# Performance work log

Hardware: AMD Instinct MI355X
Metric: run time of the kernel (lower is better)

## Reference

```python
import jax, jax.numpy as jnp
import numpy as np

M_SIGMA = 1.0 * 0.997 / 3.0  # args.m * 0.997 / 3


def setup_inputs() -> dict:
    key = jax.random.key(0)
    k1, k2 = jax.random.split(key)
    B, D = 64, 512        # batch (sketches+shapes), embedding dim
    P = 256               # points per cloud
    embeddings = jax.random.normal(k1, (B, D), dtype=jnp.float32)
    xyz = jax.random.normal(k2, (B, P, 3), dtype=jnp.float32)
    return {"embeddings": embeddings, "xyz": xyz}


def _chamfer_all_pairs(shapes):
    # shapes: [M, P, 3]. Returns cd[i, j] = chamfer(shapes[i], shapes[j]),
    # chamfer = mean_p min_q ||x_p - y_q||^2 + mean_q min_p ||x_p - y_q||^2
    sq = jnp.sum(shapes * shapes, axis=-1)                  # [M, P]
    inner = jnp.einsum('ipd,jqd->ijpq', shapes, shapes)     # [M, M, P, P]
    d2 = sq[:, None, :, None] + sq[None, :, None, :] - 2.0 * inner
    cd = jnp.min(d2, axis=3).mean(axis=2) + jnp.min(d2, axis=2).mean(axis=2)
    return cd  # [M, M]


def reference(embeddings, xyz):
    # L2-normalize embeddings along feature dim
    emb = embeddings / jnp.linalg.norm(embeddings, axis=1, keepdims=True)
    B = emb.shape[0]
    mb = B // 2
    shapes = xyz[mb:]                                       # [mb, P, 3]
    sketch_feat, shape_feat = emb[:mb], emb[mb:]            # [mb, D] each
    inner_dot = sketch_feat @ shape_feat.T                  # [mb, mb]
    cd = _chamfer_all_pairs(shapes)                         # [mb, mb]
    real_dist = (cd ** 2) / (2.0 * M_SIGMA ** 2)
    p = jax.nn.softmax(-real_dist, axis=1)
    p_hat = jax.nn.softmax(inner_dot, axis=1)               # use_softmax=True
    reg = jnp.mean(jnp.abs(p_hat - p))                      # use_KL=False
    return reg
```

## Files before the change

### kernel.cpp

```cpp
#include <hip/hip_runtime.h>
#include <math.h>


typedef float f32x2 __attribute__((ext_vector_type(2)));

__device__ __forceinline__ float waveReduceSum64(float v) {
    #pragma unroll
    for (int m = 32; m > 0; m >>= 1) v += __shfl_xor(v, m, 64);
    return v;
}

__global__ __launch_bounds__(256) void pairs_kernel(const float* __restrict__ emb,
                                                    const float* __restrict__ xyz,
                                                    float* __restrict__ cdHalf,
                                                    float* __restrict__ dots) {
    const int t = threadIdx.x;
    const int b = blockIdx.x;

    __shared__ float S[512];

    if (b < 248) {
        const int w    = t >> 6;
        const int lane = t & 63;
        const int pairIdx = __builtin_amdgcn_readfirstlane((b << 2) | w);
        const int pb  = pairIdx >> 1;
        const int dir = pairIdx & 1;
        int ii = 0, rem = pb;
        while (rem >= (31 - ii)) { rem -= (31 - ii); ++ii; }
        const int jj = ii + 1 + rem;
        const int outer = dir ? jj : ii;
        const int inner = dir ? ii : jj;

        const float* Po = xyz + (32 + outer) * 768;
        const float* Qf = xyz + (32 + inner) * 768;

        float px[4], py[4], pz[4], pp[4];
        #pragma unroll
        for (int k = 0; k < 4; ++k) {
            const float* P = Po + 3 * (lane + 64 * k);
            px[k] = P[0]; py[k] = P[1]; pz[k] = P[2];
            pp[k] = px[k] * px[k] + py[k] * py[k] + pz[k] * pz[k];
        }
        const f32x2 X01 = {-2.f * px[0], -2.f * px[1]}, X23 = {-2.f * px[2], -2.f * px[3]};
        const f32x2 Y01 = {-2.f * py[0], -2.f * py[1]}, Y23 = {-2.f * py[2], -2.f * py[3]};
        const f32x2 Z01 = {-2.f * pz[0], -2.f * pz[1]}, Z23 = {-2.f * pz[2], -2.f * pz[3]};

        f32x2 m01 = {3.4e38f, 3.4e38f}, m23 = {3.4e38f, 3.4e38f};

        #pragma unroll 8
        for (int s = 0; s < 256; ++s) {
            const float qx = Qf[3 * s];
            const float qy = Qf[3 * s + 1];
            const float qz = Qf[3 * s + 2];
            const float qw = qx * qx + qy * qy + qz * qz;
            const f32x2 QX = {qx, qx}, QY = {qy, qy}, QZ = {qz, qz}, QW = {qw, qw};
            f32x2 e01 = Z01 * QZ + QW;
            e01 = Y01 * QY + e01;
            e01 = X01 * QX + e01;
            f32x2 e23 = Z23 * QZ + QW;
            e23 = Y23 * QY + e23;
            e23 = X23 * QX + e23;
            m01.x = fminf(m01.x, e01.x); m01.y = fminf(m01.y, e01.y);
            m23.x = fminf(m23.x, e23.x); m23.y = fminf(m23.y, e23.y);
        }

        float ssum = (m01.x + pp[0]) + (m01.y + pp[1]) +
                     (m23.x + pp[2]) + (m23.y + pp[3]);
        ssum = waveReduceSum64(ssum);
        if (lane == 0) cdHalf[pairIdx] = ssum * (1.0f / 256.0f);
    } else {
        const int i = b - 248;
        float* rowi = S;
        const float* Ei = emb + i * 512;
        rowi[t]       = Ei[t];
        rowi[t + 256] = Ei[t + 256];
        __syncthreads();

        const int w    = t >> 6;
        const int lane = t & 63;

        float ni = 0.0f;
        #pragma unroll
        for (int m = 0; m < 8; ++m) { float a = rowi[lane + 64 * m]; ni += a * a; }
        ni = waveReduceSum64(ni);

        for (int j = w; j < 32; j += 4) {
            const float* Ej = emb + (32 + j) * 512;
            float dot = 0.0f, nj = 0.0f;
            #pragma unroll
            for (int m = 0; m < 8; ++m) {
                float a  = rowi[lane + 64 * m];
                float bv = Ej[lane + 64 * m];
                dot += a * bv;
                nj  += bv * bv;
            }
            dot = waveReduceSum64(dot);
            nj  = waveReduceSum64(nj);
            if (lane == 0) dots[i * 32 + j] = dot * rsqrtf(ni * nj);
        }
    }
}

__global__ __launch_bounds__(1024) void finish_kernel(const float* __restrict__ cdHalf,
                                                      const float* __restrict__ dots,
                                                      float* __restrict__ out) {
    const int t = threadIdx.x;
    const int i = t >> 5;
    const int j = t & 31;
    const float inv_denom = 1.0f / (2.0f * (0.997f / 3.0f) * (0.997f / 3.0f));

    float c;
    if (i == j) {
        c = 0.0f;
    } else {
        const int a  = min(i, j), bb = max(i, j);
        const int pb = a * 31 - (a * (a - 1)) / 2 + (bb - a - 1);
        c = cdHalf[2 * pb] + cdHalf[2 * pb + 1];
    }
    float s = -(c * c) * inv_denom;
    float h = dots[t];

    float m1 = s;
    #pragma unroll
    for (int k = 16; k > 0; k >>= 1) m1 = fmaxf(m1, __shfl_xor(m1, k, 32));
    float e1 = expf(s - m1);
    float sum1 = e1;
    #pragma unroll
    for (int k = 16; k > 0; k >>= 1) sum1 += __shfl_xor(sum1, k, 32);
    float p = e1 / sum1;

    float m2 = h;
    #pragma unroll
    for (int k = 16; k > 0; k >>= 1) m2 = fmaxf(m2, __shfl_xor(m2, k, 32));
    float e2 = expf(h - m2);
    float sum2 = e2;
    #pragma unroll
    for (int k = 16; k > 0; k >>= 1) sum2 += __shfl_xor(sum2, k, 32);
    float ph = e2 / sum2;

    float a = fabsf(ph - p);
    a = waveReduceSum64(a);

    __shared__ float red[16];
    if ((t & 63) == 0) red[t >> 6] = a;
    __syncthreads();
    if (t == 0) {
        float tot = 0.0f;
        #pragma unroll
        for (int k = 0; k < 16; ++k) tot += red[k];
        out[0] = tot * (1.0f / 1024.0f);
    }
}

extern "C" void kernel_launch(void* const* d_in, const int* in_sizes, int n_in,
                              void* d_out, int out_size, void* d_ws, size_t ws_size,
                              hipStream_t stream) {
    (void)in_sizes; (void)n_in; (void)out_size; (void)ws_size;
    const float* emb = (const float*)d_in[0];
    const float* xyz = (const float*)d_in[1];
    float* cdHalf = (float*)d_ws;
    float* dots   = cdHalf + 1024;
    float* out    = (float*)d_out;

    hipLaunchKernelGGL(pairs_kernel, dim3(280), dim3(256), 0, stream, emb, xyz, cdHalf, dots);
    hipLaunchKernelGGL(finish_kernel, dim3(1), dim3(1024), 0, stream, cdHalf, dots, out);
}
```

Measured before the change: 67.19 us.

## Split each chamfer pair across four waves with readlane broadcast of inner points

Each directed shape pair now gets its own 256-thread block. Each wave holds 64 inner points in registers and broadcasts them with readlane instead of streaming all 256 through scalar or global loads. Per-wave minima are combined across waves through shared memory before the sum reduction. This raises the wave count fourfold and shortens the serial loop, at the cost of extra barriers and LDS traffic per block.

After: 66.90 us. Within noise of the previous version (-0.4%).

```diff
diff --git a/kernel.cpp b/kernel.cpp
--- a/kernel.cpp
+++ b/kernel.cpp
@@ -10,21 +10,25 @@
     return v;
 }
 
+__device__ __forceinline__ float readlane_f(float v, int l) {
+    return __int_as_float(__builtin_amdgcn_readlane(__float_as_int(v), l));
+}
+
 __global__ __launch_bounds__(256) void pairs_kernel(const float* __restrict__ emb,
                                                     const float* __restrict__ xyz,
                                                     float* __restrict__ cdHalf,
                                                     float* __restrict__ dots) {
     const int t = threadIdx.x;
     const int b = blockIdx.x;
+    const int w    = t >> 6;
+    const int lane = t & 63;
 
-    __shared__ float S[512];
+    __shared__ __align__(16) float M[1024];
+    __shared__ float red[4];
 
-    if (b < 248) {
-        const int w    = t >> 6;
-        const int lane = t & 63;
-        const int pairIdx = __builtin_amdgcn_readfirstlane((b << 2) | w);
-        const int pb  = pairIdx >> 1;
-        const int dir = pairIdx & 1;
+    if (b < 992) {
+        const int pb  = b >> 1;
+        const int dir = b & 1;
         int ii = 0, rem = pb;
         while (rem >= (31 - ii)) { rem -= (31 - ii); ++ii; }
         const int jj = ii + 1 + rem;
@@ -32,12 +36,16 @@
         const int inner = dir ? ii : jj;
 
         const float* Po = xyz + (32 + outer) * 768;
-        const float* Qf = xyz + (32 + inner) * 768;
+        const float* Pi = xyz + (32 + inner) * 768;
+
+        const float* Q = Pi + 3 * (64 * w + lane);
+        const float qx = Q[0], qy = Q[1], qz = Q[2];
+        const float qw = qx * qx + qy * qy + qz * qz;
 
         float px[4], py[4], pz[4], pp[4];
         #pragma unroll
         for (int k = 0; k < 4; ++k) {
-            const float* P = Po + 3 * (lane + 64 * k);
+            const float* P = Po + 3 * (64 * k + lane);
             px[k] = P[0]; py[k] = P[1]; pz[k] = P[2];
             pp[k] = px[k] * px[k] + py[k] * py[k] + pz[k] * pz[k];
         }
@@ -47,37 +55,43 @@
 
         f32x2 m01 = {3.4e38f, 3.4e38f}, m23 = {3.4e38f, 3.4e38f};
 
-        #pragma unroll 8
-        for (int s = 0; s < 256; ++s) {
-            const float qx = Qf[3 * s];
-            const float qy = Qf[3 * s + 1];
-            const float qz = Qf[3 * s + 2];
-            const float qw = qx * qx + qy * qy + qz * qz;
-            const f32x2 QX = {qx, qx}, QY = {qy, qy}, QZ = {qz, qz}, QW = {qw, qw};
-            f32x2 e01 = Z01 * QZ + QW;
-            e01 = Y01 * QY + e01;
-            e01 = X01 * QX + e01;
-            f32x2 e23 = Z23 * QZ + QW;
-            e23 = Y23 * QY + e23;
-            e23 = X23 * QX + e23;
+        #pragma unroll
+        for (int k = 0; k < 64; ++k) {
+            const float sx = readlane_f(qx, k);
+            const float sy = readlane_f(qy, k);
+            const float sz = readlane_f(qz, k);
+            const float sw = readlane_f(qw, k);
+            const f32x2 SW = {sw, sw};
+            f32x2 e01 = Z01 * (f32x2){sz, sz} + SW;
+            e01 = Y01 * (f32x2){sy, sy} + e01;
+            e01 = X01 * (f32x2){sx, sx} + e01;
+            f32x2 e23 = Z23 * (f32x2){sz, sz} + SW;
+            e23 = Y23 * (f32x2){sy, sy} + e23;
+            e23 = X23 * (f32x2){sx, sx} + e23;
             m01.x = fminf(m01.x, e01.x); m01.y = fminf(m01.y, e01.y);
             m23.x = fminf(m23.x, e23.x); m23.y = fminf(m23.y, e23.y);
         }
 
-        float ssum = (m01.x + pp[0]) + (m01.y + pp[1]) +
-                     (m23.x + pp[2]) + (m23.y + pp[3]);
-        ssum = waveReduceSum64(ssum);
-        if (lane == 0) cdHalf[pairIdx] = ssum * (1.0f / 256.0f);
+        M[w * 256 +   0 + lane] = m01.x + pp[0];
+        M[w * 256 +  64 + lane] = m01.y + pp[1];
+        M[w * 256 + 128 + lane] = m23.x + pp[2];
+        M[w * 256 + 192 + lane] = m23.y + pp[3];
+        __syncthreads();
+
+        const float v = fminf(fminf(M[t], M[256 + t]),
+                              fminf(M[512 + t], M[768 + t]));
+        float s = waveReduceSum64(v);
+        if (lane == 0) red[w] = s;
+        __syncthreads();
+        if (t == 0)
+            cdHalf[b] = (red[0] + red[1] + red[2] + red[3]) * (1.0f / 256.0f);
     } else {
-        const int i = b - 248;
-        float* rowi = S;
+        const int i = b - 992;
+        float* rowi = M;
         const float* Ei = emb + i * 512;
         rowi[t]       = Ei[t];
         rowi[t + 256] = Ei[t + 256];
         __syncthreads();
-
-        const int w    = t >> 6;
-        const int lane = t & 63;
 
         float ni = 0.0f;
         #pragma unroll
@@ -162,6 +176,6 @@
     float* dots   = cdHalf + 1024;
     float* out    = (float*)d_out;
 
-    hipLaunchKernelGGL(pairs_kernel, dim3(280), dim3(256), 0, stream, emb, xyz, cdHalf, dots);
+    hipLaunchKernelGGL(pairs_kernel, dim3(1024), dim3(256), 0, stream, emb, xyz, cdHalf, dots);
     hipLaunchKernelGGL(finish_kernel, dim3(1), dim3(1024), 0, stream, cdHalf, dots, out);
 }
```
